# Performance work log

Hardware: AMD Instinct MI355X
Metric: run time of the kernel (lower is better)

The kernel has to match this reference:

```python
import jax, jax.numpy as jnp
import numpy as np

B, S, HID = 1, 2048, 2048
H, KV, D = 16, 8, 128          # heads, kv heads, head_dim
EPS = 1e-6
THETA_T, THETA_HW = 1000000.0, 10000.0
SCALE = D ** -0.5
NEG = -1e9


def _rms(x, w):
    xf = x.astype(jnp.float32)
    var = jnp.mean(xf * xf, axis=-1, keepdims=True)
    return (w * (xf * jax.lax.rsqrt(var + EPS))).astype(x.dtype)


def _rope_cs(pos, theta, half_dim):
    # Module builds RoPE with head_dim = 2*half_dim then takes every-other freq:
    # exponents arange(0, 2*half_dim, 4) / (2*half_dim)  -> half_dim//2 freqs
    dim2 = 2 * half_dim
    inv_freq = 1.0 / theta ** (jnp.arange(0, dim2, 4, dtype=jnp.float32) / dim2)
    freqs = pos.astype(jnp.float32)[:, None] * inv_freq[None, :]   # [S, half_dim//2]
    emb = jnp.concatenate([freqs, freqs], axis=-1)                 # [S, half_dim]
    return jnp.cos(emb), jnp.sin(emb)


def _rot_half(x):
    d = x.shape[-1] // 2
    return jnp.concatenate([-x[..., d:], x[..., :d]], axis=-1)


def _apply_rope(q, k, cos, sin):
    cos = cos[None, None]  # [1,1,S,dim]
    sin = sin[None, None]
    return q * cos + _rot_half(q) * sin, k * cos + _rot_half(k) * sin


def setup_inputs() -> dict:
    key = jax.random.key(0)
    ks = jax.random.split(key, 10)
    hidden_states = jax.random.normal(ks[0], (B, S, HID), jnp.float32)
    indexes = jax.random.randint(ks[1], (3, S), 0, S)
    causal = jnp.tril(jnp.ones((S, S), bool))
    attention_mask = jnp.where(causal, 0.0, NEG).astype(jnp.float32)[None, None]
    qkv_w = jax.random.normal(ks[2], ((H + 2 * KV) * D, HID), jnp.float32) * 0.02
    qkv_b = jax.random.normal(ks[3], ((H + 2 * KV) * D,), jnp.float32) * 0.02
    o_w = jax.random.normal(ks[4], (HID, H * D), jnp.float32) * 0.02
    o_b = jax.random.normal(ks[5], (HID,), jnp.float32) * 0.02
    q_norm_w = jnp.ones((D // 2,), jnp.float32)
    k_norm_w = jnp.ones((D // 2,), jnp.float32)
    q_norm_hw_w = jnp.ones((D // 2,), jnp.float32)
    k_norm_hw_w = jnp.ones((D // 2,), jnp.float32)
    return dict(hidden_states=hidden_states, indexes=indexes, attention_mask=attention_mask,
                qkv_w=qkv_w, qkv_b=qkv_b, o_w=o_w, o_b=o_b,
                q_norm_w=q_norm_w, k_norm_w=k_norm_w,
                q_norm_hw_w=q_norm_hw_w, k_norm_hw_w=k_norm_hw_w)


def reference(hidden_states, indexes, attention_mask, qkv_w, qkv_b, o_w, o_b,
              q_norm_w, k_norm_w, q_norm_hw_w, k_norm_hw_w):
    b, s, _ = hidden_states.shape
    qkv = hidden_states @ qkv_w.T + qkv_b
    q, k, v = jnp.split(qkv, [H * D, H * D + KV * D], axis=-1)
    q = q.reshape(b, s, H, D)
    k = k.reshape(b, s, KV, D)
    v = v.reshape(b, s, KV, D)

    # split head_dim into time half and hw half
    q_t, q_hw = jnp.split(q, 2, axis=-1)
    k_t, k_hw = jnp.split(k, 2, axis=-1)
    q_t = jnp.swapaxes(_rms(q_t, q_norm_w), 1, 2)       # [B,H,S,D/2]
    k_t = jnp.swapaxes(_rms(k_t, k_norm_w), 1, 2)
    q_hw = jnp.swapaxes(_rms(q_hw, q_norm_hw_w), 1, 2)
    k_hw = jnp.swapaxes(_rms(k_hw, k_norm_hw_w), 1, 2)
    q_h, q_ww = jnp.split(q_hw, 2, axis=-1)             # [B,H,S,D/4]
    k_h, k_ww = jnp.split(k_hw, 2, axis=-1)

    cos_t, sin_t = _rope_cs(indexes[0], THETA_T, D // 2)
    q_t, k_t = _apply_rope(q_t, k_t, cos_t, sin_t)
    cos_h, sin_h = _rope_cs(indexes[1], THETA_HW, D // 4)
    q_h, k_h = _apply_rope(q_h, k_h, cos_h, sin_h)
    cos_w, sin_w = _rope_cs(indexes[2], THETA_HW, D // 4)
    q_ww, k_ww = _apply_rope(q_ww, k_ww, cos_w, sin_w)

    query = jnp.concatenate([q_t, q_h, q_ww], axis=-1)  # [B,H,S,D]
    keyst = jnp.concatenate([k_t, k_h, k_ww], axis=-1)  # [B,KV,S,D]
    value = jnp.swapaxes(v, 1, 2)                       # [B,KV,S,D]

    n_rep = H // KV
    keyst = jnp.repeat(keyst, n_rep, axis=1)
    value = jnp.repeat(value, n_rep, axis=1)

    scores = jnp.einsum('bhsd,bhtd->bhst', query, keyst) * SCALE + attention_mask
    probs = jax.nn.softmax(scores.astype(jnp.float32), axis=-1).astype(query.dtype)
    attn = jnp.einsum('bhst,bhtd->bhsd', probs, value)
    attn = jnp.swapaxes(attn, 1, 2).reshape(b, s, H * D)
    return attn @ o_w.T + o_b
```

## Files before the change

kernel.cpp:

```cpp
#include <hip/hip_runtime.h>

typedef __bf16 bf16;
typedef __bf16 bf16x4 __attribute__((ext_vector_type(4)));
typedef __bf16 bf16x8 __attribute__((ext_vector_type(8)));
typedef float f32x4 __attribute__((ext_vector_type(4)));

#define S_LEN 2048
#define HIDDEN 2048
#define NH 16
#define NKV 8
#define HD 128
#define QKV_N 4096

__device__ __forceinline__ void async_load16(const void* g, void* l) {
  __builtin_amdgcn_global_load_lds((const __attribute__((address_space(1))) unsigned int*)g,
                                   (__attribute__((address_space(3))) unsigned int*)l,
                                   16, 0, 0);
}

template <int C>
__device__ __forceinline__ float dpp_f(float x) {
  return __builtin_bit_cast(float, __builtin_amdgcn_mov_dpp(
      __builtin_bit_cast(int, x), C, 0xF, 0xF, true));
}
__device__ __forceinline__ float rowmax16(float x) {
  x = fmaxf(x, dpp_f<0x128>(x));
  x = fmaxf(x, dpp_f<0x124>(x));
  x = fmaxf(x, dpp_f<0x122>(x));
  x = fmaxf(x, dpp_f<0x121>(x));
  return x;
}
__device__ __forceinline__ float rowsum16(float x) {
  x += dpp_f<0x128>(x);
  x += dpp_f<0x124>(x);
  x += dpp_f<0x122>(x);
  x += dpp_f<0x121>(x);
  return x;
}

__global__ __launch_bounds__(256)
void cvt_f32_bf16(const float* __restrict__ src, bf16* __restrict__ dst, int n) {
  int i = (blockIdx.x * 256 + threadIdx.x) * 4;
  if (i < n) {
    float4 v = *(const float4*)(src + i);
    bf16x4 o = {(bf16)v.x, (bf16)v.y, (bf16)v.z, (bf16)v.w};
    *(bf16x4*)(dst + i) = o;
  }
}

template <int WRITE_BF16>
__global__ __launch_bounds__(256)
void gemm_bt(const bf16* __restrict__ A, const bf16* __restrict__ B,
             const float* __restrict__ bias, void* __restrict__ Cout,
             int M, int N, int K) {
  __shared__ bf16 As[128 * 32];
  __shared__ bf16 Bs[128 * 32];
  const int tid = threadIdx.x;
  const int w = tid >> 6, lane = tid & 63;
  const int quad = lane >> 4, l15 = lane & 15;
  const int wm = w >> 1, wn = w & 1;
  const int m0 = blockIdx.y * 128, n0 = blockIdx.x * 128;

  f32x4 acc[4][4];
#pragma unroll
  for (int i = 0; i < 4; i++)
#pragma unroll
    for (int j = 0; j < 4; j++) acc[i][j] = (f32x4){0.f, 0.f, 0.f, 0.f};

  const int crow = lane >> 2;
  const int ccol = (lane & 3) * 8;

  for (int k0 = 0; k0 < K; k0 += 32) {
    __syncthreads();
#pragma unroll
    for (int q = 0; q < 2; q++) {
      int c = 2 * w + q;
      async_load16(A + (size_t)(m0 + c * 16 + crow) * K + k0 + ccol, (char*)As + c * 1024);
      async_load16(B + (size_t)(n0 + c * 16 + crow) * K + k0 + ccol, (char*)Bs + c * 1024);
    }
    __syncthreads();
    bf16x8 af[4], bfr[4];
#pragma unroll
    for (int i = 0; i < 4; i++)
      af[i] = *(const bf16x8*)(As + (wm * 64 + i * 16 + l15) * 32 + quad * 8);
#pragma unroll
    for (int j = 0; j < 4; j++)
      bfr[j] = *(const bf16x8*)(Bs + (wn * 64 + j * 16 + l15) * 32 + quad * 8);
#pragma unroll
    for (int i = 0; i < 4; i++)
#pragma unroll
      for (int j = 0; j < 4; j++)
        acc[i][j] = __builtin_amdgcn_mfma_f32_16x16x32_bf16(af[i], bfr[j], acc[i][j], 0, 0, 0);
  }

#pragma unroll
  for (int i = 0; i < 4; i++) {
#pragma unroll
    for (int j = 0; j < 4; j++) {
      int col = n0 + wn * 64 + j * 16 + l15;
      float bv = bias[col];
#pragma unroll
      for (int r = 0; r < 4; r++) {
        int row = m0 + wm * 64 + i * 16 + quad * 4 + r;
        float v = acc[i][j][r] + bv;
        if (WRITE_BF16)
          ((bf16*)Cout)[(size_t)row * N + col] = (bf16)v;
        else
          ((float*)Cout)[(size_t)row * N + col] = v;
      }
    }
  }
}

__global__ __launch_bounds__(256)
void gemm_bt64(const bf16* __restrict__ A, const bf16* __restrict__ B,
               const float* __restrict__ bias, float* __restrict__ Cout,
               int M, int N, int K) {
  __shared__ bf16 As[128 * 32];
  __shared__ bf16 Bs[64 * 32];
  const int tid = threadIdx.x;
  const int w = tid >> 6, lane = tid & 63;
  const int quad = lane >> 4, l15 = lane & 15;
  const int m0 = blockIdx.y * 128, n0 = blockIdx.x * 64;

  f32x4 acc[2][4];
#pragma unroll
  for (int i = 0; i < 2; i++)
#pragma unroll
    for (int j = 0; j < 4; j++) acc[i][j] = (f32x4){0.f, 0.f, 0.f, 0.f};

  const int crow = lane >> 2;
  const int ccol = (lane & 3) * 8;

  for (int k0 = 0; k0 < K; k0 += 32) {
    __syncthreads();
#pragma unroll
    for (int q = 0; q < 2; q++) {
      int c = 2 * w + q;
      async_load16(A + (size_t)(m0 + c * 16 + crow) * K + k0 + ccol, (char*)As + c * 1024);
    }
    async_load16(B + (size_t)(n0 + w * 16 + crow) * K + k0 + ccol, (char*)Bs + w * 1024);
    __syncthreads();
    bf16x8 af[2], bfr[4];
#pragma unroll
    for (int i = 0; i < 2; i++)
      af[i] = *(const bf16x8*)(As + (w * 32 + i * 16 + l15) * 32 + quad * 8);
#pragma unroll
    for (int j = 0; j < 4; j++)
      bfr[j] = *(const bf16x8*)(Bs + (j * 16 + l15) * 32 + quad * 8);
#pragma unroll
    for (int i = 0; i < 2; i++)
#pragma unroll
      for (int j = 0; j < 4; j++)
        acc[i][j] = __builtin_amdgcn_mfma_f32_16x16x32_bf16(af[i], bfr[j], acc[i][j], 0, 0, 0);
  }

#pragma unroll
  for (int i = 0; i < 2; i++) {
#pragma unroll
    for (int j = 0; j < 4; j++) {
      int col = n0 + j * 16 + l15;
      float bv = bias[col];
#pragma unroll
      for (int r = 0; r < 4; r++) {
        int row = m0 + w * 32 + i * 16 + quad * 4 + r;
        Cout[(size_t)row * N + col] = acc[i][j][r] + bv;
      }
    }
  }
}

__global__ __launch_bounds__(128)
void normrope(const bf16* __restrict__ qkv, const int* __restrict__ idx,
              const float* __restrict__ qnw, const float* __restrict__ knw,
              const float* __restrict__ qnhw, const float* __restrict__ knhw,
              bf16* __restrict__ Qb, bf16* __restrict__ Kb) {
  const int s = blockIdx.x;
  const int y = blockIdx.y;
  const int d = threadIdx.x;

  const bool isq = (y < 16);
  const int off = isq ? (y * HD + d) : (2048 + (y - 16) * HD + d);
  float x = (float)qkv[(size_t)s * QKV_N + off];

  float ss = x * x;
#pragma unroll
  for (int o = 32; o; o >>= 1) ss += __shfl_xor(ss, o);
  float inv = rsqrtf(ss * (1.f / 64.f) + 1e-6f);
  const float* wt = (d < 64) ? (isq ? qnw : knw) : (isq ? qnhw : knhw);
  float yn = x * inv * wt[d & 63];

  float pos, invf;
  int xorm;
  bool firsthalf;
  if (d < 64) {
    pos = (float)idx[s];
    int i = d & 31;
    invf = exp2f(-(float)i * 0.6228615177913804f);
    xorm = 32;
    firsthalf = (d < 32);
  } else {
    int j = d - 64;
    int region = j >> 5;
    pos = (float)idx[(1 + region) * S_LEN + s];
    int i = j & 15;
    invf = exp2f(-(float)i * 0.8304820237218406f);
    xorm = 16;
    firsthalf = ((j & 31) < 16);
  }
  float ang = pos * invf;
  float si, co;
  sincosf(ang, &si, &co);
  float partner = __shfl_xor(yn, xorm);
  float outv = firsthalf ? (yn * co - partner * si) : (yn * co + partner * si);

  if (isq)
    Qb[((size_t)y * S_LEN + s) * HD + d] = (bf16)outv;
  else
    Kb[((size_t)(y - 16) * S_LEN + s) * HD + d] = (bf16)outv;
}

__global__ __launch_bounds__(256)
void vtrans(const bf16* __restrict__ qkv, bf16* __restrict__ VT) {
  __shared__ bf16 T[64][72];
  const int tid = threadIdx.x;
  const int s0 = blockIdx.x * 64, d0 = blockIdx.y * 64, kv = blockIdx.z;
#pragma unroll
  for (int it = 0; it < 2; it++) {
    int r = (tid >> 3) + it * 32;
    int c = (tid & 7) * 8;
    bf16x8 v = *(const bf16x8*)(qkv + (size_t)(s0 + r) * QKV_N + 3072 + kv * HD + d0 + c);
    *(bf16x8*)(&T[r][c]) = v;
  }
  __syncthreads();
#pragma unroll
  for (int it = 0; it < 2; it++) {
    int r = (tid >> 3) + it * 32;
    int c = (tid & 7) * 8;
    bf16x8 o;
#pragma unroll
    for (int j = 0; j < 8; j++) o[j] = T[c + j][r];
    *(bf16x8*)(VT + ((size_t)kv * HD + d0 + r) * S_LEN + s0 + c) = o;
  }
}

__global__ __launch_bounds__(256)
void attn_fused(const bf16* __restrict__ Qb, const bf16* __restrict__ Kb,
                const bf16* __restrict__ VT, bf16* __restrict__ attnO) {
  __shared__ bf16 Kbuf[2][8192];
  __shared__ bf16 Vbuf[8192];
  __shared__ __align__(16) bf16 Ps[4][16][72];
  const int tid = threadIdx.x;
  const int w = tid >> 6, lane = tid & 63;
  const int quad = lane >> 4, l15 = lane & 15;
  const int b = blockIdx.x;
  const int h = b & 15;
  const int g = b >> 4;
  const int qb64 = (g < 16) ? (31 - g) : (g - 16);
  const int nT = qb64 + 1;
  const int qr0 = qb64 * 64 + w * 16;
  const int kv = h >> 1;

  const bf16* Qg = Qb + (size_t)h * S_LEN * HD;
  const bf16* Kg = Kb + (size_t)kv * S_LEN * HD;
  const bf16* Vg = VT + (size_t)kv * HD * S_LEN;

  const bf16* ksrc = Kg + (size_t)(w * 16 + l15) * HD + quad * 8;
  const bf16* vsrc = Vg + (size_t)(2 * w * 16 + l15) * S_LEN + quad * 8;

  bf16x8 aq[4];
#pragma unroll
  for (int kc = 0; kc < 4; kc++)
    aq[kc] = *(const bf16x8*)(Qg + (size_t)(qr0 + l15) * HD + kc * 32 + quad * 8);

  float m2[4], li[4];
  f32x4 Oacc[8];
#pragma unroll
  for (int r = 0; r < 4; r++) { m2[r] = -1e30f; li[r] = 0.f; }
#pragma unroll
  for (int dt = 0; dt < 8; dt++) Oacc[dt] = (f32x4){0.f, 0.f, 0.f, 0.f};

  const float SC2 = 0.12751745f;

#pragma unroll
  for (int kc = 0; kc < 4; kc++)
    async_load16(ksrc + kc * 32, (char*)Kbuf[0] + (w * 4 + kc) * 1024);

  for (int tt = 0; tt < nT; ++tt) {
    const int t0 = tt << 6;
    const int cur = tt & 1;
    const bool more = (tt + 1 < nT);
    __asm__ __volatile__("s_waitcnt vmcnt(0)" ::: "memory");
    __syncthreads();

#pragma unroll
    for (int e = 0; e < 2; e++)
#pragma unroll
      for (int half = 0; half < 2; half++)
        async_load16(vsrc + (size_t)e * 16 * S_LEN + t0 + half * 32,
                     (char*)Vbuf + (half * 8 + 2 * w + e) * 1024);
    if (more) {
#pragma unroll
      for (int kc = 0; kc < 4; kc++)
        async_load16(ksrc + (size_t)(t0 + 64) * HD + kc * 32,
                     (char*)Kbuf[cur ^ 1] + (w * 4 + kc) * 1024);
    }

    f32x4 sacc[4];
#pragma unroll
    for (int nt = 0; nt < 4; nt++) {
      sacc[nt] = (f32x4){0.f, 0.f, 0.f, 0.f};
#pragma unroll
      for (int kc = 0; kc < 4; kc++) {
        bf16x8 bk = *(const bf16x8*)((const char*)Kbuf[cur] + (nt * 4 + kc) * 1024 + lane * 16);
        sacc[nt] = __builtin_amdgcn_mfma_f32_16x16x32_bf16(aq[kc], bk, sacc[nt], 0, 0, 0);
      }
    }

    const bool full = (t0 + 64 <= qr0);
#pragma unroll
    for (int r = 0; r < 4; r++) {
      const int mrow = qr0 + quad * 4 + r;
      float s0 = sacc[0][r] * SC2, s1 = sacc[1][r] * SC2;
      float s2 = sacc[2][r] * SC2, s3 = sacc[3][r] * SC2;
      if (!full) {
        int cb = t0 + l15;
        if (cb > mrow) s0 = -1e30f;
        if (cb + 16 > mrow) s1 = -1e30f;
        if (cb + 32 > mrow) s2 = -1e30f;
        if (cb + 48 > mrow) s3 = -1e30f;
      }
      float mx = rowmax16(fmaxf(fmaxf(s0, s1), fmaxf(s2, s3)));
      float mnew = fmaxf(m2[r], mx);
      float alpha = exp2f(m2[r] - mnew);
      float p0 = exp2f(s0 - mnew), p1 = exp2f(s1 - mnew);
      float p2 = exp2f(s2 - mnew), p3 = exp2f(s3 - mnew);
      float rs = rowsum16((p0 + p1) + (p2 + p3));
      li[r] = li[r] * alpha + rs;
      m2[r] = mnew;
#pragma unroll
      for (int dt = 0; dt < 8; dt++) Oacc[dt][r] *= alpha;
      Ps[w][quad * 4 + r][l15] = (bf16)p0;
      Ps[w][quad * 4 + r][16 + l15] = (bf16)p1;
      Ps[w][quad * 4 + r][32 + l15] = (bf16)p2;
      Ps[w][quad * 4 + r][48 + l15] = (bf16)p3;
    }
    __asm__ __volatile__("s_waitcnt lgkmcnt(0)" ::: "memory");
    if (more)
      __asm__ __volatile__("s_waitcnt vmcnt(4)" ::: "memory");
    else
      __asm__ __volatile__("s_waitcnt vmcnt(0)" ::: "memory");

#pragma unroll
    for (int half = 0; half < 2; half++) {
      bf16x8 ap = *(const bf16x8*)(&Ps[w][l15][half * 32 + quad * 8]);
#pragma unroll
      for (int dt = 0; dt < 8; dt++) {
        bf16x8 bv = *(const bf16x8*)((const char*)Vbuf + (half * 8 + dt) * 1024 + lane * 16);
        Oacc[dt] = __builtin_amdgcn_mfma_f32_16x16x32_bf16(ap, bv, Oacc[dt], 0, 0, 0);
      }
    }
  }

#pragma unroll
  for (int r = 0; r < 4; r++) {
    float invl = 1.f / li[r];
    int srow = qr0 + quad * 4 + r;
#pragma unroll
    for (int dt = 0; dt < 8; dt++)
      attnO[(size_t)srow * HIDDEN + h * HD + dt * 16 + l15] = (bf16)(Oacc[dt][r] * invl);
  }
}

extern "C" void kernel_launch(void* const* d_in, const int* in_sizes, int n_in,
                              void* d_out, int out_size, void* d_ws, size_t ws_size,
                              hipStream_t stream) {
  const float* hidden = (const float*)d_in[0];
  const int* idx = (const int*)d_in[1];
  const float* qkv_w = (const float*)d_in[3];
  const float* qkv_b = (const float*)d_in[4];
  const float* o_w = (const float*)d_in[5];
  const float* o_b = (const float*)d_in[6];
  const float* qnw = (const float*)d_in[7];
  const float* knw = (const float*)d_in[8];
  const float* qnhw = (const float*)d_in[9];
  const float* knhw = (const float*)d_in[10];

  char* ws = (char*)d_ws;
  bf16* hB   = (bf16*)(ws);
  bf16* qwB  = (bf16*)(ws + (8u << 20));
  bf16* qkvB = (bf16*)(ws + (24u << 20));
  bf16* Qb   = (bf16*)(ws + (40u << 20));
  bf16* Kb   = (bf16*)(ws + (48u << 20));
  bf16* VT   = (bf16*)(ws + (52u << 20));
  bf16* owB  = hB;
  bf16* attn = qwB;

  cvt_f32_bf16<<<HIDDEN * S_LEN / 1024, 256, 0, stream>>>(hidden, hB, HIDDEN * S_LEN);
  cvt_f32_bf16<<<QKV_N * HIDDEN / 1024, 256, 0, stream>>>(qkv_w, qwB, QKV_N * HIDDEN);

  gemm_bt<1><<<dim3(QKV_N / 128, S_LEN / 128), 256, 0, stream>>>(
      hB, qwB, qkv_b, qkvB, S_LEN, QKV_N, HIDDEN);

  cvt_f32_bf16<<<HIDDEN * HIDDEN / 1024, 256, 0, stream>>>(o_w, owB, HIDDEN * HIDDEN);

  normrope<<<dim3(S_LEN, 24), 128, 0, stream>>>(qkvB, idx, qnw, knw, qnhw, knhw, Qb, Kb);
  vtrans<<<dim3(S_LEN / 64, HD / 64, NKV), 256, 0, stream>>>(qkvB, VT);

  attn_fused<<<512, 256, 0, stream>>>(Qb, Kb, VT, attn);

  gemm_bt64<<<dim3(HIDDEN / 64, S_LEN / 128), 256, 0, stream>>>(
      attn, owB, o_b, (float*)d_out, S_LEN, HIDDEN, HIDDEN);
}
```

Before: 312.1 us.

## Deepen GEMM K-tiles, merge conversions, fold softmax scale into Q, fast sincos

Both GEMM kernels now stage 64-wide K slices per barrier instead of 32. The shared-memory tiles are laid out as contiguous 16x32 MFMA fragments, so each lane reads at lane*16, and an explicit vmcnt wait precedes the barrier. This halves the number of sync points per K and should cut LDS bank conflicts. The two f32->bf16 conversions are merged into one launch. The attention scale is folded into Q in normrope, removing per-score multiplies. sincosf is replaced by the less accurate __sinf/__cosf, which risks precision on large rope angles, and the pre-bf16 scaling of Q changes rounding slightly.

Result: slower. 321.0 us (+2.9%).

```diff
diff --git a/kernel.cpp b/kernel.cpp
--- a/kernel.cpp
+++ b/kernel.cpp
@@ -39,6 +39,19 @@
 }
 
 __global__ __launch_bounds__(256)
+void cvt2(const float* __restrict__ a, bf16* __restrict__ da, int na,
+          const float* __restrict__ b, bf16* __restrict__ db) {
+  int i = (blockIdx.x * 256 + threadIdx.x) * 4;
+  const float* s;
+  bf16* d;
+  if (i < na) { s = a + i; d = da + i; }
+  else        { s = b + (i - na); d = db + (i - na); }
+  float4 v = *(const float4*)s;
+  bf16x4 o = {(bf16)v.x, (bf16)v.y, (bf16)v.z, (bf16)v.w};
+  *(bf16x4*)d = o;
+}
+
+__global__ __launch_bounds__(256)
 void cvt_f32_bf16(const float* __restrict__ src, bf16* __restrict__ dst, int n) {
   int i = (blockIdx.x * 256 + threadIdx.x) * 4;
   if (i < n) {
@@ -53,8 +66,8 @@
 void gemm_bt(const bf16* __restrict__ A, const bf16* __restrict__ B,
              const float* __restrict__ bias, void* __restrict__ Cout,
              int M, int N, int K) {
-  __shared__ bf16 As[128 * 32];
-  __shared__ bf16 Bs[128 * 32];
+  __shared__ bf16 As[8192];
+  __shared__ bf16 Bs[8192];
   const int tid = threadIdx.x;
   const int w = tid >> 6, lane = tid & 63;
   const int quad = lane >> 4, l15 = lane & 15;
@@ -67,30 +80,33 @@
 #pragma unroll
     for (int j = 0; j < 4; j++) acc[i][j] = (f32x4){0.f, 0.f, 0.f, 0.f};
 
-  const int crow = lane >> 2;
-  const int ccol = (lane & 3) * 8;
-
-  for (int k0 = 0; k0 < K; k0 += 32) {
+  for (int k0 = 0; k0 < K; k0 += 64) {
     __syncthreads();
 #pragma unroll
-    for (int q = 0; q < 2; q++) {
-      int c = 2 * w + q;
-      async_load16(A + (size_t)(m0 + c * 16 + crow) * K + k0 + ccol, (char*)As + c * 1024);
-      async_load16(B + (size_t)(n0 + c * 16 + crow) * K + k0 + ccol, (char*)Bs + c * 1024);
-    }
+    for (int q = 0; q < 4; q++) {
+      int i = 2 * w + (q >> 1), kc = q & 1;
+      async_load16(A + (size_t)(m0 + i * 16 + l15) * K + k0 + kc * 32 + quad * 8,
+                   (char*)As + (4 * w + q) * 1024);
+      async_load16(B + (size_t)(n0 + i * 16 + l15) * K + k0 + kc * 32 + quad * 8,
+                   (char*)Bs + (4 * w + q) * 1024);
+    }
+    __asm__ __volatile__("s_waitcnt vmcnt(0)" ::: "memory");
     __syncthreads();
-    bf16x8 af[4], bfr[4];
-#pragma unroll
-    for (int i = 0; i < 4; i++)
-      af[i] = *(const bf16x8*)(As + (wm * 64 + i * 16 + l15) * 32 + quad * 8);
-#pragma unroll
-    for (int j = 0; j < 4; j++)
-      bfr[j] = *(const bf16x8*)(Bs + (wn * 64 + j * 16 + l15) * 32 + quad * 8);
-#pragma unroll
-    for (int i = 0; i < 4; i++)
+#pragma unroll
+    for (int kc = 0; kc < 2; kc++) {
+      bf16x8 af[4], bfr[4];
+#pragma unroll
+      for (int i = 0; i < 4; i++)
+        af[i] = *(const bf16x8*)((const char*)As + ((wm * 4 + i) * 2 + kc) * 1024 + lane * 16);
 #pragma unroll
       for (int j = 0; j < 4; j++)
-        acc[i][j] = __builtin_amdgcn_mfma_f32_16x16x32_bf16(af[i], bfr[j], acc[i][j], 0, 0, 0);
+        bfr[j] = *(const bf16x8*)((const char*)Bs + ((wn * 4 + j) * 2 + kc) * 1024 + lane * 16);
+#pragma unroll
+      for (int i = 0; i < 4; i++)
+#pragma unroll
+        for (int j = 0; j < 4; j++)
+          acc[i][j] = __builtin_amdgcn_mfma_f32_16x16x32_bf16(af[i], bfr[j], acc[i][j], 0, 0, 0);
+    }
   }
 
 #pragma unroll
@@ -116,8 +132,8 @@
 void gemm_bt64(const bf16* __restrict__ A, const bf16* __restrict__ B,
                const float* __restrict__ bias, float* __restrict__ Cout,
                int M, int N, int K) {
-  __shared__ bf16 As[128 * 32];
-  __shared__ bf16 Bs[64 * 32];
+  __shared__ bf16 As[8192];
+  __shared__ bf16 Bs[4096];
   const int tid = threadIdx.x;
   const int w = tid >> 6, lane = tid & 63;
   const int quad = lane >> 4, l15 = lane & 15;
@@ -129,30 +145,36 @@
 #pragma unroll
     for (int j = 0; j < 4; j++) acc[i][j] = (f32x4){0.f, 0.f, 0.f, 0.f};
 
-  const int crow = lane >> 2;
-  const int ccol = (lane & 3) * 8;
-
-  for (int k0 = 0; k0 < K; k0 += 32) {
+  for (int k0 = 0; k0 < K; k0 += 64) {
     __syncthreads();
 #pragma unroll
+    for (int q = 0; q < 4; q++) {
+      int i = 2 * w + (q >> 1), kc = q & 1;
+      async_load16(A + (size_t)(m0 + i * 16 + l15) * K + k0 + kc * 32 + quad * 8,
+                   (char*)As + (4 * w + q) * 1024);
+    }
+#pragma unroll
     for (int q = 0; q < 2; q++) {
-      int c = 2 * w + q;
-      async_load16(A + (size_t)(m0 + c * 16 + crow) * K + k0 + ccol, (char*)As + c * 1024);
-    }
-    async_load16(B + (size_t)(n0 + w * 16 + crow) * K + k0 + ccol, (char*)Bs + w * 1024);
+      async_load16(B + (size_t)(n0 + w * 16 + l15) * K + k0 + q * 32 + quad * 8,
+                   (char*)Bs + (2 * w + q) * 1024);
+    }
+    __asm__ __volatile__("s_waitcnt vmcnt(0)" ::: "memory");
     __syncthreads();
-    bf16x8 af[2], bfr[4];
-#pragma unroll
-    for (int i = 0; i < 2; i++)
-      af[i] = *(const bf16x8*)(As + (w * 32 + i * 16 + l15) * 32 + quad * 8);
-#pragma unroll
-    for (int j = 0; j < 4; j++)
-      bfr[j] = *(const bf16x8*)(Bs + (j * 16 + l15) * 32 + quad * 8);
-#pragma unroll
-    for (int i = 0; i < 2; i++)
+#pragma unroll
+    for (int kc = 0; kc < 2; kc++) {
+      bf16x8 af[2], bfr[4];
+#pragma unroll
+      for (int i = 0; i < 2; i++)
+        af[i] = *(const bf16x8*)((const char*)As + ((2 * w + i) * 2 + kc) * 1024 + lane * 16);
 #pragma unroll
       for (int j = 0; j < 4; j++)
-        acc[i][j] = __builtin_amdgcn_mfma_f32_16x16x32_bf16(af[i], bfr[j], acc[i][j], 0, 0, 0);
+        bfr[j] = *(const bf16x8*)((const char*)Bs + (j * 2 + kc) * 1024 + lane * 16);
+#pragma unroll
+      for (int i = 0; i < 2; i++)
+#pragma unroll
+        for (int j = 0; j < 4; j++)
+          acc[i][j] = __builtin_amdgcn_mfma_f32_16x16x32_bf16(af[i], bfr[j], acc[i][j], 0, 0, 0);
+    }
   }
 
 #pragma unroll
@@ -209,13 +231,12 @@
     firsthalf = ((j & 31) < 16);
   }
   float ang = pos * invf;
-  float si, co;
-  sincosf(ang, &si, &co);
+  float si = __sinf(ang), co = __cosf(ang);
   float partner = __shfl_xor(yn, xorm);
   float outv = firsthalf ? (yn * co - partner * si) : (yn * co + partner * si);
 
   if (isq)
-    Qb[((size_t)y * S_LEN + s) * HD + d] = (bf16)outv;
+    Qb[((size_t)y * S_LEN + s) * HD + d] = (bf16)(outv * 0.12751745f);
   else
     Kb[((size_t)(y - 16) * S_LEN + s) * HD + d] = (bf16)outv;
 }
@@ -280,8 +301,6 @@
 #pragma unroll
   for (int dt = 0; dt < 8; dt++) Oacc[dt] = (f32x4){0.f, 0.f, 0.f, 0.f};
 
-  const float SC2 = 0.12751745f;
-
 #pragma unroll
   for (int kc = 0; kc < 4; kc++)
     async_load16(ksrc + kc * 32, (char*)Kbuf[0] + (w * 4 + kc) * 1024);
@@ -321,8 +340,8 @@
 #pragma unroll
     for (int r = 0; r < 4; r++) {
       const int mrow = qr0 + quad * 4 + r;
-      float s0 = sacc[0][r] * SC2, s1 = sacc[1][r] * SC2;
-      float s2 = sacc[2][r] * SC2, s3 = sacc[3][r] * SC2;
+      float s0 = sacc[0][r], s1 = sacc[1][r];
+      float s2 = sacc[2][r], s3 = sacc[3][r];
       if (!full) {
         int cb = t0 + l15;
         if (cb > mrow) s0 = -1e30f;
@@ -396,8 +415,9 @@
   bf16* owB  = hB;
   bf16* attn = qwB;
 
-  cvt_f32_bf16<<<HIDDEN * S_LEN / 1024, 256, 0, stream>>>(hidden, hB, HIDDEN * S_LEN);
-  cvt_f32_bf16<<<QKV_N * HIDDEN / 1024, 256, 0, stream>>>(qkv_w, qwB, QKV_N * HIDDEN);
+  const int nH = HIDDEN * S_LEN;
+  const int nW = QKV_N * HIDDEN;
+  cvt2<<<(nH + nW) / 1024, 256, 0, stream>>>(hidden, hB, nH, qkv_w, qwB);
 
   gemm_bt<1><<<dim3(QKV_N / 128, S_LEN / 128), 256, 0, stream>>>(
       hB, qwB, qkv_b, qkvB, S_LEN, QKV_N, HIDDEN);
```
